# Kernel optimization log

Measured on AMD Instinct MI355X. Metric: run time of the kernel, lower is better.

## Reference

```python
import jax, jax.numpy as jnp
import numpy as np

DIM = 512
HEADS = 8
DIM_HEAD = 64
DIM_INNER = HEADS * DIM_HEAD
SCALE = DIM_HEAD ** -0.5


def setup_inputs() -> dict:
    key = jax.random.key(0)
    ks = jax.random.split(key, 8)
    b, n = 2, 1024
    x = jax.random.normal(ks[0], (b, n, DIM), dtype=jnp.float32)
    w = lambda k, i, o: jax.random.normal(k, (i, o), dtype=jnp.float32) * 0.02
    return {
        'x': x,
        'w_q_u': w(ks[1], DIM, DIM_INNER),
        'w_k_u': w(ks[2], DIM, DIM_INNER),
        'w_v_u': w(ks[3], DIM, DIM_INNER),
        'w_q_c': w(ks[4], DIM, DIM_INNER),
        'w_k_c': w(ks[5], DIM, DIM_INNER),
        'w_v_c': w(ks[6], DIM, DIM_INNER),
        'w_out': w(ks[7], DIM_INNER, DIM),
    }


def reference(x, w_q_u, w_k_u, w_v_u, w_q_c, w_k_c, w_v_c, w_out):
    b, n, _ = x.shape

    def proj(w):  # [b,n,dim] -> [b,h,n,d]
        return (x @ w).reshape(b, n, HEADS, DIM_HEAD).transpose(0, 2, 1, 3)

    q_u, k_u, v_u = proj(w_q_u), proj(w_k_u), proj(w_v_u)
    q_c, k_c, v_c = proj(w_q_c), proj(w_k_c), proj(w_v_c)

    idx = jnp.arange(n)
    causal = idx[:, None] >= idx[None, :]  # tril ones (binary causal mask)

    # term1 = (q_c @ v_u^T) * scale, zeroed above diagonal
    term1 = jnp.einsum('bhid,bhjd->bhij', q_c, v_u) * SCALE
    term1 = term1 * causal.astype(term1.dtype)

    # sigmoid term: (q_u @ k_u^T)*scale with lookahead mask tril(-inf, diag=0)
    logits_u = jnp.einsum('bhid,bhjd->bhij', q_u, k_u) * SCALE
    sig = jax.nn.sigmoid(jnp.where(causal, -jnp.inf, logits_u))

    # S_u[i,k] = sum_j term1[i,j] * sig[k,j]
    S_u = jnp.einsum('bhij,bhkj->bhik', term1, sig)

    # S_c: causal-masked QK
    S_c = jnp.einsum('bhid,bhjd->bhij', q_c, k_c) * SCALE
    S_c = jnp.where(causal, S_c, -jnp.inf)

    final_scores = S_c - jax.nn.silu(S_u)
    attn = jax.nn.softmax(final_scores, axis=-1)
    out = jnp.einsum('bhij,bhjd->bhid', attn, v_c)  # [b,h,n,d]
    out = out.transpose(0, 2, 1, 3).reshape(b, n, DIM_INNER)
    return out @ w_out
```

## Files before the change

kernel.cpp:

```cpp
#include <hip/hip_runtime.h>
#include <math.h>


typedef __bf16 bf16x8 __attribute__((ext_vector_type(8)));
typedef float f32x4 __attribute__((ext_vector_type(4)));

#define SCALE 0.125f

#define GLL(g, l) __builtin_amdgcn_global_load_lds(                         \
    (const __attribute__((address_space(1))) void*)(g),                     \
    (__attribute__((address_space(3))) void*)(l), 16, 0, 0)

__device__ __forceinline__ unsigned short f2bf(float f){
  unsigned int x = __builtin_bit_cast(unsigned int, f);
  unsigned int r = (x + 0x7fffu + ((x >> 16) & 1u)) >> 16;
  return (unsigned short)r;
}
__device__ __forceinline__ float bf2f(unsigned short u){
  unsigned int x = ((unsigned int)u) << 16;
  return __builtin_bit_cast(float, x);
}
__device__ __forceinline__ f32x4 mfma16(bf16x8 a, bf16x8 b, f32x4 c){
  return __builtin_amdgcn_mfma_f32_16x16x32_bf16(a, b, c, 0, 0, 0);
}
__device__ __forceinline__ bf16x8 ld8(const unsigned short* p){
  return *(const bf16x8*)p;
}

__global__ __launch_bounds__(256) void k_prep(
    const float* __restrict__ x,
    const float* __restrict__ w0, const float* __restrict__ w1,
    const float* __restrict__ w2, const float* __restrict__ w3,
    const float* __restrict__ w4, const float* __restrict__ w5,
    const float* __restrict__ w6,
    unsigned short* __restrict__ xb, unsigned short* __restrict__ wT){
  int t = threadIdx.x;
  if (blockIdx.x < 1024){
    int i = blockIdx.x * 256 + t;
    float4 v = ((const float4*)x)[i];
    ushort4 o; o.x = f2bf(v.x); o.y = f2bf(v.y); o.z = f2bf(v.z); o.w = f2bf(v.w);
    ((ushort4*)xb)[i] = o;
    return;
  }
  __shared__ float lds[64 * 65];
  int bx = blockIdx.x - 1024;
  int mat = bx >> 6, tile = bx & 63, tr = tile >> 3, tc = tile & 7;
  int k0 = tr * 64, c0 = tc * 64;
  const float* src;
  switch (mat){
    case 0: src = w0; break; case 1: src = w1; break; case 2: src = w2; break;
    case 3: src = w3; break; case 4: src = w4; break; case 5: src = w5; break;
    default: src = w6; break;
  }
#pragma unroll
  for (int i = 0; i < 4; ++i){
    int r = (t >> 4) + i * 16, c4 = (t & 15) * 4;
    float4 v = *(const float4*)(src + (size_t)(k0 + r) * 512 + c0 + c4);
    lds[r * 65 + c4 + 0] = v.x; lds[r * 65 + c4 + 1] = v.y;
    lds[r * 65 + c4 + 2] = v.z; lds[r * 65 + c4 + 3] = v.w;
  }
  __syncthreads();
  unsigned short* dst = wT + (size_t)mat * 262144;
#pragma unroll
  for (int i = 0; i < 4; ++i){
    int oc = (t >> 4) + i * 16;
    int kq = (t & 15) * 4;
    ushort4 o;
    o.x = f2bf(lds[(kq + 0) * 65 + oc]);
    o.y = f2bf(lds[(kq + 1) * 65 + oc]);
    o.z = f2bf(lds[(kq + 2) * 65 + oc]);
    o.w = f2bf(lds[(kq + 3) * 65 + oc]);
    *(ushort4*)(dst + (size_t)(c0 + oc) * 512 + k0 + kq) = o;
  }
}

__global__ __launch_bounds__(256) void k_proj(
    const unsigned short* __restrict__ xb, const unsigned short* __restrict__ wT,
    unsigned short* __restrict__ P){
  __shared__ unsigned short sA[128 * 32], sB[128 * 32];
  int t = threadIdx.x, lane = t & 63, l16 = lane & 15, quad = lane >> 4;
  int w = t >> 6, wm = w >> 1, wn = w & 1;
  int bx = blockIdx.x;
  int mt = bx / 24, nt = bx - mt * 24;
  int M0 = mt * 128, N0 = nt * 128;
  int matb = N0 >> 9;
  int nin = N0 & 511;
  int srow = (lane >> 2), scol = (lane & 3) * 8;
  const unsigned short* gA = xb + (size_t)(M0 + w*32 + srow) * 512 + scol;
  const unsigned short* gB = wT + (size_t)matb * 262144
                               + (size_t)(nin + w*32 + srow) * 512 + scol;
  unsigned short* lA = sA + (w*32) * 32;
  unsigned short* lB = sB + (w*32) * 32;
  f32x4 acc[4][4] = {};
  for (int k0 = 0; k0 < 512; k0 += 32){
    GLL(gA + k0,            lA);
    GLL(gA + k0 + 16*512,   lA + 16*32);
    GLL(gB + k0,            lB);
    GLL(gB + k0 + 16*512,   lB + 16*32);
    __syncthreads();
    bf16x8 aw[4], ax[4];
#pragma unroll
    for (int fi = 0; fi < 4; ++fi)
      aw[fi] = *(const bf16x8*)(sB + (wn*64 + fi*16 + l16) * 32 + quad * 8);
#pragma unroll
    for (int mi = 0; mi < 4; ++mi)
      ax[mi] = *(const bf16x8*)(sA + (wm*64 + mi*16 + l16) * 32 + quad * 8);
#pragma unroll
    for (int fi = 0; fi < 4; ++fi)
#pragma unroll
      for (int mi = 0; mi < 4; ++mi)
        acc[fi][mi] = mfma16(aw[fi], ax[mi], acc[fi][mi]);
    __syncthreads();
  }
#pragma unroll
  for (int fi = 0; fi < 4; ++fi)
#pragma unroll
    for (int mi = 0; mi < 4; ++mi){
      int row = M0 + wm*64 + mi*16 + l16;
      int b_ = row >> 10, n_ = row & 1023;
      int c0 = N0 + wn*64 + fi*16 + quad*4;
      int h = (c0 & 511) >> 6, d = c0 & 63;
      int bh = b_*8 + h;
      ushort4 o;
      o.x = f2bf(acc[fi][mi][0]); o.y = f2bf(acc[fi][mi][1]);
      o.z = f2bf(acc[fi][mi][2]); o.w = f2bf(acc[fi][mi][3]);
      *(ushort4*)(P + (size_t)(matb*16 + bh) * 65536 + (size_t)n_ * 64 + d) = o;
    }
}

__global__ __launch_bounds__(256) void k_qk_vct(
    const unsigned short* __restrict__ P,
    unsigned short* __restrict__ term1, unsigned short* __restrict__ sig,
    unsigned short* __restrict__ vcT){
  __shared__ unsigned short lds[64 * 72];
  int t = threadIdx.x;
  if (blockIdx.x < 256){
    int bh = blockIdx.x >> 4, nt = blockIdx.x & 15;
    int N0 = nt * 64;
    const unsigned short* src = P + (size_t)(5*16 + bh) * 65536 + (size_t)N0 * 64;
#pragma unroll
    for (int it = 0; it < 2; ++it){
      int id = it * 256 + t;
      int r = id >> 3, c8 = (id & 7) * 8;
      ushort4 v0 = *(const ushort4*)(src + r * 64 + c8);
      ushort4 v1 = *(const ushort4*)(src + r * 64 + c8 + 4);
      *(ushort4*)(lds + r * 72 + c8) = v0;
      *(ushort4*)(lds + r * 72 + c8 + 4) = v1;
    }
    __syncthreads();
    unsigned short* dst = vcT + (size_t)bh * 65536;
#pragma unroll
    for (int it = 0; it < 2; ++it){
      int id = it * 256 + t;
      int dd = id >> 3, n8 = (id & 7) * 8;
      ushort4 a, b;
      a.x = lds[(n8+0)*72 + dd]; a.y = lds[(n8+1)*72 + dd];
      a.z = lds[(n8+2)*72 + dd]; a.w = lds[(n8+3)*72 + dd];
      b.x = lds[(n8+4)*72 + dd]; b.y = lds[(n8+5)*72 + dd];
      b.z = lds[(n8+6)*72 + dd]; b.w = lds[(n8+7)*72 + dd];
      *(ushort4*)(dst + (size_t)dd * 1024 + N0 + n8) = a;
      *(ushort4*)(dst + (size_t)dd * 1024 + N0 + n8 + 4) = b;
    }
    return;
  }
  int gw = ((blockIdx.x - 256) * 256 + t) >> 6;
  int lane = t & 63, l16 = lane & 15, quad = lane >> 4;
  int bhm = gw / 576;
  int idx = gw - bhm * 576;
  int bh = bhm >> 1, mat = bhm & 1;
  int B = 0;
  while (idx >= 8 * (B + 1) * (B + 2)) ++B;
  int r2 = idx - 8 * B * (B + 1);
  int per = 2 * (B + 1);
  int mt_in = r2 / per, sub = r2 - mt_in * per;
  int m0 = (B * 8 + mt_in) * 16, n0 = sub * 64;
  if (mat){ m0 = 1008 - m0; n0 = 960 - n0; }
  unsigned short* out = (mat ? sig : term1) + (size_t)bh * 1048576;
  int row = m0 + l16;
  bool zero_tile = mat ? (n0 + 63 <= m0) : (n0 > m0 + 15);
  if (zero_tile){
    ushort4 z = {0, 0, 0, 0};
#pragma unroll
    for (int f = 0; f < 4; ++f)
      *(ushort4*)(out + (size_t)row * 1024 + n0 + f*16 + quad*4) = z;
    return;
  }
  const unsigned short* A  = P + (size_t)((mat ? 0 : 3)*16 + bh) * 65536;
  const unsigned short* Bt = P + (size_t)((mat ? 1 : 2)*16 + bh) * 65536;
  f32x4 acc[4] = {};
  for (int k0 = 0; k0 < 64; k0 += 32){
    bf16x8 bi = ld8(A + (size_t)(m0 + l16) * 64 + k0 + quad * 8);
#pragma unroll
    for (int f = 0; f < 4; ++f){
      bf16x8 aj = ld8(Bt + (size_t)(n0 + f*16 + l16) * 64 + k0 + quad * 8);
      acc[f] = mfma16(aj, bi, acc[f]);
    }
  }
#pragma unroll
  for (int f = 0; f < 4; ++f){
    int c0 = n0 + f*16 + quad*4;
    ushort4 o;
#pragma unroll
    for (int r = 0; r < 4; ++r){
      int col = c0 + r;
      float v = acc[f][r] * SCALE;
      unsigned short res;
      if (mat == 0) res = (col <= row) ? f2bf(v) : (unsigned short)0;
      else          res = (col >  row) ? f2bf(1.f / (1.f + expf(-v))) : (unsigned short)0;
      ((unsigned short*)&o)[r] = res;
    }
    *(ushort4*)(out + (size_t)row * 1024 + c0) = o;
  }
}

__global__ __launch_bounds__(256) void k_scores(
    const unsigned short* __restrict__ P, const unsigned short* __restrict__ term1,
    const unsigned short* __restrict__ sig, unsigned short* __restrict__ finb){
  __shared__ unsigned short sA[128 * 32], sB[128 * 32];
  int t = threadIdx.x;
  int bh = blockIdx.x & 15, tt = blockIdx.x >> 4;
  int k = 1, T = 0;
  while (tt >= T + k){ T += k; ++k; }
  int delta = 8 - k;
  int tj = tt - T, ti = tj + delta;
  int M0 = ti * 128, N0 = tj * 128;
  size_t sbase = (size_t)bh * 1048576;
  int lane = t & 63, l16 = lane & 15, quad = lane >> 4;
  int w = t >> 6, wm = w >> 1, wn = w & 1;
  int srow = (lane >> 2), scol = (lane & 3) * 8;
  unsigned short* lA = sA + (w*32) * 32;
  unsigned short* lB = sB + (w*32) * 32;
  f32x4 acc_u[4][4] = {};
  f32x4 acc_c[4][4] = {};
  {
    const unsigned short* gA = term1 + sbase + (size_t)(M0 + w*32 + srow) * 1024 + scol;
    const unsigned short* gB = sig   + sbase + (size_t)(N0 + w*32 + srow) * 1024 + scol;
    int steps = (delta + 1) * 4;
    for (int s = 0; s < steps; ++s){
      int j0 = N0 + s * 32;
      GLL(gA + j0,             lA);
      GLL(gA + j0 + 16*1024,   lA + 16*32);
      GLL(gB + j0,             lB);
      GLL(gB + j0 + 16*1024,   lB + 16*32);
      __syncthreads();
      bf16x8 af[4], bfr[4];
#pragma unroll
      for (int mi = 0; mi < 4; ++mi)
        af[mi] = *(const bf16x8*)(sA + (wm*64 + mi*16 + l16) * 32 + quad * 8);
#pragma unroll
      for (int fi = 0; fi < 4; ++fi)
        bfr[fi] = *(const bf16x8*)(sB + (wn*64 + fi*16 + l16) * 32 + quad * 8);
#pragma unroll
      for (int fi = 0; fi < 4; ++fi)
#pragma unroll
        for (int mi = 0; mi < 4; ++mi)
          acc_u[fi][mi] = mfma16(bfr[fi], af[mi], acc_u[fi][mi]);
      __syncthreads();
    }
  }
  {
    const unsigned short* Qc = P + (size_t)(3*16 + bh) * 65536;
    const unsigned short* Kc = P + (size_t)(4*16 + bh) * 65536;
#pragma unroll
    for (int k0 = 0; k0 < 64; k0 += 32){
      bf16x8 af[4], bfr[4];
#pragma unroll
      for (int mi = 0; mi < 4; ++mi)
        af[mi] = ld8(Qc + (size_t)(M0 + wm*64 + mi*16 + l16) * 64 + k0 + quad * 8);
#pragma unroll
      for (int fi = 0; fi < 4; ++fi)
        bfr[fi] = ld8(Kc + (size_t)(N0 + wn*64 + fi*16 + l16) * 64 + k0 + quad * 8);
#pragma unroll
      for (int fi = 0; fi < 4; ++fi)
#pragma unroll
        for (int mi = 0; mi < 4; ++mi)
          acc_c[fi][mi] = mfma16(bfr[fi], af[mi], acc_c[fi][mi]);
    }
  }
  unsigned short* out = finb + sbase;
#pragma unroll
  for (int fi = 0; fi < 4; ++fi)
#pragma unroll
    for (int mi = 0; mi < 4; ++mi){
      int row = M0 + wm*64 + mi*16 + l16;
      int c0 = N0 + wn*64 + fi*16 + quad*4;
      ushort4 o;
#pragma unroll
      for (int r = 0; r < 4; ++r){
        float su = acc_u[fi][mi][r];
        float v = acc_c[fi][mi][r] * SCALE - su / (1.f + expf(-su));
        ((unsigned short*)&o)[r] = f2bf(v);
      }
      *(ushort4*)(out + (size_t)row * 1024 + c0) = o;
    }
}

__global__ __launch_bounds__(256) void k_pv_soft(
    const unsigned short* __restrict__ finb, const unsigned short* __restrict__ vcT,
    unsigned short* __restrict__ O){
  __shared__ __align__(16) unsigned char smem[16 * 1032 * 2];
  unsigned short* lp = (unsigned short*)smem;
  float* red = (float*)smem;
  int t = threadIdx.x;
  int bh = blockIdx.x & 15, mt = 63 - (blockIdx.x >> 4);
  int m0 = mt * 16;
  int kceil = ((m0 + 16 + 31) >> 5) << 5;
  {
    int rl = t >> 4, sub = t & 15;
    int rloc = m0 + rl;
    const unsigned short* p = finb + (size_t)bh * 1048576 + (size_t)rloc * 1024;
    float v[8][8];
    float m = -INFINITY;
#pragma unroll
    for (int i = 0; i < 8; ++i){
      int c8 = (sub + 16*i) * 8;
      if (c8 < kceil){
        ushort4 u0 = *(const ushort4*)(p + c8);
        ushort4 u1 = *(const ushort4*)(p + c8 + 4);
        float vv[8] = {bf2f(u0.x), bf2f(u0.y), bf2f(u0.z), bf2f(u0.w),
                       bf2f(u1.x), bf2f(u1.y), bf2f(u1.z), bf2f(u1.w)};
#pragma unroll
        for (int e = 0; e < 8; ++e){
          v[i][e] = (c8 + e <= rloc) ? vv[e] : -INFINITY;
          m = fmaxf(m, v[i][e]);
        }
      }
    }
#pragma unroll
    for (int off = 1; off < 16; off <<= 1) m = fmaxf(m, __shfl_xor(m, off));
    float s = 0.f;
#pragma unroll
    for (int i = 0; i < 8; ++i){
      int c8 = (sub + 16*i) * 8;
      if (c8 < kceil){
#pragma unroll
        for (int e = 0; e < 8; ++e){
          v[i][e] = expf(v[i][e] - m);
          s += v[i][e];
        }
      }
    }
#pragma unroll
    for (int off = 1; off < 16; off <<= 1) s += __shfl_xor(s, off);
    float inv = 1.f / s;
#pragma unroll
    for (int i = 0; i < 8; ++i){
      int c8 = (sub + 16*i) * 8;
      if (c8 < kceil){
        ushort4 o0, o1;
        o0.x = f2bf(v[i][0] * inv); o0.y = f2bf(v[i][1] * inv);
        o0.z = f2bf(v[i][2] * inv); o0.w = f2bf(v[i][3] * inv);
        o1.x = f2bf(v[i][4] * inv); o1.y = f2bf(v[i][5] * inv);
        o1.z = f2bf(v[i][6] * inv); o1.w = f2bf(v[i][7] * inv);
        *(ushort4*)(lp + rl * 1032 + c8) = o0;
        *(ushort4*)(lp + rl * 1032 + c8 + 4) = o1;
      }
    }
  }
  __syncthreads();
  int lane = t & 63, l16 = lane & 15, quad = lane >> 4, w = t >> 6;
  const unsigned short* Bt = vcT + (size_t)bh * 65536;
  int ktot = kceil >> 5;
  int per = (ktot + 3) >> 2;
  int s0 = w * per, s1 = min(s0 + per, ktot);
  f32x4 acc[4] = {};
  for (int s = s0; s < s1; ++s){
    int k0 = s * 32;
    bf16x8 a = *(const bf16x8*)(lp + l16 * 1032 + k0 + quad * 8);
#pragma unroll
    for (int fi = 0; fi < 4; ++fi){
      bf16x8 b = ld8(Bt + (size_t)(fi*16 + l16) * 1024 + k0 + quad * 8);
      acc[fi] = mfma16(a, b, acc[fi]);
    }
  }
  __syncthreads();
#pragma unroll
  for (int fi = 0; fi < 4; ++fi)
#pragma unroll
    for (int r = 0; r < 4; ++r)
      red[w * 1024 + (quad*4 + r) * 64 + fi*16 + l16] = acc[fi][r];
  __syncthreads();
  float4 a0 = ((const float4*)(red + 0*1024))[t];
  float4 a1 = ((const float4*)(red + 1*1024))[t];
  float4 a2 = ((const float4*)(red + 2*1024))[t];
  float4 a3 = ((const float4*)(red + 3*1024))[t];
  ushort4 o;
  o.x = f2bf(a0.x + a1.x + a2.x + a3.x);
  o.y = f2bf(a0.y + a1.y + a2.y + a3.y);
  o.z = f2bf(a0.z + a1.z + a2.z + a3.z);
  o.w = f2bf(a0.w + a1.w + a2.w + a3.w);
  int e = t * 4, row = e >> 6, col = e & 63;
  *(ushort4*)(O + (size_t)bh * 65536 + (size_t)(m0 + row) * 64 + col) = o;
}

__global__ __launch_bounds__(256) void k_out(
    const unsigned short* __restrict__ O, const unsigned short* __restrict__ woT,
    float* __restrict__ out){
  __shared__ float red[4][1024];
  int t = threadIdx.x, lane = t & 63, l16 = lane & 15, quad = lane >> 4, w = t >> 6;
  int mt = blockIdx.x >> 3, nt = blockIdx.x & 7;
  int m0 = mt * 16, n0 = nt * 64;
  int r_ = m0 + l16, b_ = r_ >> 10, n_ = r_ & 1023;
  f32x4 acc[4] = {};
#pragma unroll
  for (int s = 0; s < 4; ++s){
    int kk = w * 128 + s * 32 + quad * 8;
    int h = kk >> 6, dd = kk & 63;
    bf16x8 a = ld8(O + (size_t)(b_*8 + h) * 65536 + (size_t)n_ * 64 + dd);
#pragma unroll
    for (int fi = 0; fi < 4; ++fi){
      bf16x8 b = ld8(woT + (size_t)(n0 + fi*16 + l16) * 512 + kk);
      acc[fi] = mfma16(a, b, acc[fi]);
    }
  }
#pragma unroll
  for (int fi = 0; fi < 4; ++fi)
#pragma unroll
    for (int r = 0; r < 4; ++r)
      red[w][(quad*4 + r) * 64 + fi*16 + l16] = acc[fi][r];
  __syncthreads();
  float4 a0 = ((const float4*)red[0])[t];
  float4 a1 = ((const float4*)red[1])[t];
  float4 a2 = ((const float4*)red[2])[t];
  float4 a3 = ((const float4*)red[3])[t];
  float4 o;
  o.x = a0.x + a1.x + a2.x + a3.x;
  o.y = a0.y + a1.y + a2.y + a3.y;
  o.z = a0.z + a1.z + a2.z + a3.z;
  o.w = a0.w + a1.w + a2.w + a3.w;
  int e = t * 4, row = e >> 6, col = e & 63;
  *(float4*)(out + (size_t)(m0 + row) * 512 + n0 + col) = o;
}

extern "C" void kernel_launch(void* const* d_in, const int* in_sizes, int n_in,
                              void* d_out, int out_size, void* d_ws, size_t ws_size,
                              hipStream_t stream){
  const float* x = (const float*)d_in[0];
  float* out = (float*)d_out;
  unsigned short* ws = (unsigned short*)d_ws;

  unsigned short* wT    = ws;
  unsigned short* xb    = wT    + (size_t)7  * 262144;
  unsigned short* P     = xb    + (size_t)1048576;
  unsigned short* vcT   = P     + (size_t)96 * 65536;
  unsigned short* term1 = vcT   + (size_t)16 * 65536;
  unsigned short* sig   = term1 + (size_t)16 * 1048576;
  unsigned short* O     = sig   + (size_t)16 * 1048576;
  unsigned short* finb  = O     + (size_t)16 * 65536;

  k_prep<<<1472, 256, 0, stream>>>(
      x,
      (const float*)d_in[1], (const float*)d_in[2], (const float*)d_in[3],
      (const float*)d_in[4], (const float*)d_in[5], (const float*)d_in[6],
      (const float*)d_in[7], xb, wT);
  k_proj<<<384, 256, 0, stream>>>(xb, wT, P);
  k_qk_vct<<<4864, 256, 0, stream>>>(P, term1, sig, vcT);
  k_scores<<<576, 256, 0, stream>>>(P, term1, sig, finb);
  k_pv_soft<<<1024, 256, 0, stream>>>(finb, vcT, O);
  k_out<<<1024, 256, 0, stream>>>(O, wT + (size_t)6 * 262144, out);
}
```

Before: 176.7 us.

## Retile term1/sig QK kernel to 128x128 LDS tiles over triangular blocks only

Replaces the one-wave-per-16x64-tile QK computation for term1 and sig with 256-thread blocks. Each block computes a 128x128 tile, staging Q/K through LDS with global_load_lds and running a 4x4 MFMA fragment grid per wave. Only the 36 lower/upper-triangular tiles per matrix per head are launched, so the old zero-writes for fully masked tiles are gone. This cuts redundant global loads and roughly halves the output stores. The catch is that later kernels must never read the now-unwritten masked regions of term1 and sig.

```diff
diff --git a/kernel.cpp b/kernel.cpp
--- a/kernel.cpp
+++ b/kernel.cpp
@@ -132,9 +132,9 @@
     const unsigned short* __restrict__ P,
     unsigned short* __restrict__ term1, unsigned short* __restrict__ sig,
     unsigned short* __restrict__ vcT){
-  __shared__ unsigned short lds[64 * 72];
   int t = threadIdx.x;
   if (blockIdx.x < 256){
+    __shared__ unsigned short lds[64 * 72];
     int bh = blockIdx.x >> 4, nt = blockIdx.x & 15;
     int N0 = nt * 64;
     const unsigned short* src = P + (size_t)(5*16 + bh) * 65536 + (size_t)N0 * 64;
@@ -163,54 +163,70 @@
     }
     return;
   }
-  int gw = ((blockIdx.x - 256) * 256 + t) >> 6;
+  __shared__ unsigned short sA[128 * 32], sB[128 * 32];
+  int id = blockIdx.x - 256;
+  int bh = id & 15, tt = id >> 4;
+  int mat = (tt >= 36);
+  int tl = mat ? tt - 36 : tt;
+  int ti = 0;
+  while (tl >= ti + 1){ tl -= ti + 1; ++ti; }
+  int tj = tl;
+  int R0, C0;
+  const unsigned short *Asrc, *Bsrc;
+  if (!mat){ R0 = ti * 128; C0 = tj * 128;
+             Asrc = P + (size_t)(3*16 + bh) * 65536;
+             Bsrc = P + (size_t)(2*16 + bh) * 65536; }
+  else     { R0 = tj * 128; C0 = ti * 128;
+             Asrc = P + (size_t)(0*16 + bh) * 65536;
+             Bsrc = P + (size_t)(1*16 + bh) * 65536; }
   int lane = t & 63, l16 = lane & 15, quad = lane >> 4;
-  int bhm = gw / 576;
-  int idx = gw - bhm * 576;
-  int bh = bhm >> 1, mat = bhm & 1;
-  int B = 0;
-  while (idx >= 8 * (B + 1) * (B + 2)) ++B;
-  int r2 = idx - 8 * B * (B + 1);
-  int per = 2 * (B + 1);
-  int mt_in = r2 / per, sub = r2 - mt_in * per;
-  int m0 = (B * 8 + mt_in) * 16, n0 = sub * 64;
-  if (mat){ m0 = 1008 - m0; n0 = 960 - n0; }
+  int w = t >> 6, wm = w >> 1, wn = w & 1;
+  int srow = lane >> 2, scol = (lane & 3) * 8;
+  const unsigned short* gA = Asrc + (size_t)(R0 + w*32 + srow) * 64 + scol;
+  const unsigned short* gB = Bsrc + (size_t)(C0 + w*32 + srow) * 64 + scol;
+  unsigned short* lA = sA + (w*32) * 32;
+  unsigned short* lB = sB + (w*32) * 32;
+  f32x4 acc[4][4] = {};
+#pragma unroll
+  for (int k0 = 0; k0 < 64; k0 += 32){
+    GLL(gA + k0,           lA);
+    GLL(gA + k0 + 16*64,   lA + 16*32);
+    GLL(gB + k0,           lB);
+    GLL(gB + k0 + 16*64,   lB + 16*32);
+    __syncthreads();
+    bf16x8 af[4], bfr[4];
+#pragma unroll
+    for (int mi = 0; mi < 4; ++mi)
+      af[mi] = *(const bf16x8*)(sA + (wm*64 + mi*16 + l16) * 32 + quad * 8);
+#pragma unroll
+    for (int fi = 0; fi < 4; ++fi)
+      bfr[fi] = *(const bf16x8*)(sB + (wn*64 + fi*16 + l16) * 32 + quad * 8);
+#pragma unroll
+    for (int fi = 0; fi < 4; ++fi)
+#pragma unroll
+      for (int mi = 0; mi < 4; ++mi)
+        acc[fi][mi] = mfma16(bfr[fi], af[mi], acc[fi][mi]);
+    __syncthreads();
+  }
   unsigned short* out = (mat ? sig : term1) + (size_t)bh * 1048576;
-  int row = m0 + l16;
-  bool zero_tile = mat ? (n0 + 63 <= m0) : (n0 > m0 + 15);
-  if (zero_tile){
-    ushort4 z = {0, 0, 0, 0};
-#pragma unroll
-    for (int f = 0; f < 4; ++f)
-      *(ushort4*)(out + (size_t)row * 1024 + n0 + f*16 + quad*4) = z;
-    return;
-  }
-  const unsigned short* A  = P + (size_t)((mat ? 0 : 3)*16 + bh) * 65536;
-  const unsigned short* Bt = P + (size_t)((mat ? 1 : 2)*16 + bh) * 65536;
-  f32x4 acc[4] = {};
-  for (int k0 = 0; k0 < 64; k0 += 32){
-    bf16x8 bi = ld8(A + (size_t)(m0 + l16) * 64 + k0 + quad * 8);
-#pragma unroll
-    for (int f = 0; f < 4; ++f){
-      bf16x8 aj = ld8(Bt + (size_t)(n0 + f*16 + l16) * 64 + k0 + quad * 8);
-      acc[f] = mfma16(aj, bi, acc[f]);
-    }
-  }
-#pragma unroll
-  for (int f = 0; f < 4; ++f){
-    int c0 = n0 + f*16 + quad*4;
-    ushort4 o;
-#pragma unroll
-    for (int r = 0; r < 4; ++r){
-      int col = c0 + r;
-      float v = acc[f][r] * SCALE;
-      unsigned short res;
-      if (mat == 0) res = (col <= row) ? f2bf(v) : (unsigned short)0;
-      else          res = (col >  row) ? f2bf(1.f / (1.f + expf(-v))) : (unsigned short)0;
-      ((unsigned short*)&o)[r] = res;
-    }
-    *(ushort4*)(out + (size_t)row * 1024 + c0) = o;
-  }
+#pragma unroll
+  for (int fi = 0; fi < 4; ++fi)
+#pragma unroll
+    for (int mi = 0; mi < 4; ++mi){
+      int row = R0 + wm*64 + mi*16 + l16;
+      int c0 = C0 + wn*64 + fi*16 + quad*4;
+      ushort4 o;
+#pragma unroll
+      for (int r = 0; r < 4; ++r){
+        int col = c0 + r;
+        float v = acc[fi][mi][r] * SCALE;
+        unsigned short res;
+        if (!mat) res = (col <= row) ? f2bf(v) : (unsigned short)0;
+        else      res = (col >  row) ? f2bf(1.f / (1.f + expf(-v))) : (unsigned short)0;
+        ((unsigned short*)&o)[r] = res;
+      }
+      *(ushort4*)(out + (size_t)row * 1024 + c0) = o;
+    }
 }
 
 __global__ __launch_bounds__(256) void k_scores(
@@ -454,7 +470,7 @@
       (const float*)d_in[4], (const float*)d_in[5], (const float*)d_in[6],
       (const float*)d_in[7], xb, wT);
   k_proj<<<384, 256, 0, stream>>>(xb, wT, P);
-  k_qk_vct<<<4864, 256, 0, stream>>>(P, term1, sig, vcT);
+  k_qk_vct<<<1408, 256, 0, stream>>>(P, term1, sig, vcT);
   k_scores<<<576, 256, 0, stream>>>(P, term1, sig, finb);
   k_pv_soft<<<1024, 256, 0, stream>>>(finb, vcT, O);
   k_out<<<1024, 256, 0, stream>>>(O, wT + (size_t)6 * 262144, out);
```

New measurement: 171.8 us. 2.8% less time.
